# Performance work log

Hardware: AMD Instinct MI355X
Metric: run time of the kernel (lower is better)

Reference implementation:

```python
import jax, jax.numpy as jnp
import numpy as np

N_NODES = 50000
N_EDGES = 800000
IN_FEAT = 64
HID = 128
NUM_CLASSES = 32


def _glorot(key, shape):
    fan_in, fan_out = shape[0], shape[1]
    lim = jnp.sqrt(6.0 / (fan_in + fan_out))
    return jax.random.uniform(key, shape, jnp.float32, -lim, lim)


def setup_inputs() -> dict:
    key = jax.random.key(0)
    ks = jax.random.split(key, 8)
    x = jax.random.normal(ks[0], (N_NODES, IN_FEAT), dtype=jnp.float32)
    edge_index = jax.random.randint(ks[1], (2, N_EDGES), 0, N_NODES, dtype=jnp.int64 if jax.config.jax_enable_x64 else jnp.int32)
    W1 = _glorot(ks[2], (IN_FEAT, HID))
    b1 = jnp.zeros((HID,), jnp.float32)
    W2 = _glorot(ks[3], (HID, NUM_CLASSES))
    b2 = jnp.zeros((NUM_CLASSES,), jnp.float32)
    Wc = _glorot(ks[4], (NUM_CLASSES, NUM_CLASSES))
    bc = jnp.zeros((NUM_CLASSES,), jnp.float32)
    return {"x": x, "edge_index": edge_index, "W1": W1, "b1": b1,
            "W2": W2, "b2": b2, "Wc": Wc, "bc": bc}


def _gcn_conv(x, src, dst, norm, W, b):
    # x' = scatter_add(norm * gather(xW, src), dst) + b   (PyG GCNConv, self-loops included in src/dst)
    h = x @ W                                   # [N, out]
    msg = h[src] * norm[:, None]                # [E+N, out] gather + scale
    out = jax.ops.segment_sum(msg, dst, num_segments=N_NODES)  # scatter-add
    return out + b


def reference(x, edge_index, W1, b1, W2, b2, Wc, bc):
    # add self-loops (PyG GCNConv default add_self_loops=True)
    loops = jnp.arange(N_NODES, dtype=edge_index.dtype)
    src = jnp.concatenate([edge_index[0], loops])
    dst = jnp.concatenate([edge_index[1], loops])
    # symmetric normalization: deg over targets of A + I
    deg = jax.ops.segment_sum(jnp.ones_like(src, dtype=x.dtype), dst, num_segments=N_NODES)
    dinv = jnp.where(deg > 0, jax.lax.rsqrt(deg), 0.0)
    norm = dinv[src] * dinv[dst]                # [E+N]

    h = _gcn_conv(x, src, dst, norm, W1, b1)
    h = jax.nn.relu(h)                          # dropout p=0.0 -> identity
    h = _gcn_conv(h, src, dst, norm, W2, b2)
    out = h @ Wc + bc
    return (out, h)
```

## Files before the change

### kernel.cpp

```cpp
#include <hip/hip_runtime.h>


static constexpr int N  = 50000;
static constexpr int E  = 800000;
static constexpr int F0 = 64;
static constexpr int F1 = 128;
static constexpr int F2 = 32;

static constexpr int BSH    = 7;
static constexpr int BNODES = 128;
static constexpr int BMASK  = 127;
static constexpr int NBUK   = 392;
static constexpr int NSEG   = 4;
static constexpr int SEGCAP = 768;
static constexpr int BCAP   = NSEG * SEGCAP;
static constexpr int CHUNK  = 4096;
static constexpr int NCHUNK = 196;

__device__ __forceinline__ unsigned int f2bf(float f) {
  unsigned int u = __float_as_uint(f);
  return (u + 0x7fffu + ((u >> 16) & 1u)) >> 16;
}
__device__ __forceinline__ float bflo(unsigned int u) {
  return __uint_as_float(u << 16);
}
__device__ __forceinline__ float bfhi(unsigned int u) {
  return __uint_as_float(u & 0xffff0000u);
}

__global__ __launch_bounds__(512) void k_bucket(const int* __restrict__ src,
    const int* __restrict__ dst, int* __restrict__ gcur,
    unsigned int* __restrict__ ebuf) {
  __shared__ int hl[NBUK];
  int t = threadIdx.x, c = blockIdx.x;
  const int sub = c & (NSEG - 1);
  for (int i = t; i < NBUK; i += 512) hl[i] = 0;
  __syncthreads();
  int e0 = c * CHUNK, m = min(CHUNK, E - e0);
  int dreg[8];
  #pragma unroll
  for (int k = 0; k < 8; ++k) {
    int i = t + k * 512;
    if (i < m) {
      int d = dst[e0 + i];
      dreg[k] = d;
      atomicAdd(&hl[d >> BSH], 1);
    }
  }
  __syncthreads();
  for (int i = t; i < NBUK; i += 512) {
    int cc = hl[i];
    int rbase = (cc > 0) ? atomicAdd(&gcur[(i * NSEG + sub) * 16], cc) : 0;
    hl[i] = i * BCAP + sub * SEGCAP + rbase;
  }
  __syncthreads();
  #pragma unroll
  for (int k = 0; k < 8; ++k) {
    int i = t + k * 512;
    if (i < m) {
      int d = dreg[k], s = src[e0 + i];
      int pos = atomicAdd(&hl[d >> BSH], 1);
      ebuf[pos] = (unsigned int)s | ((unsigned int)(d & BMASK) << 16);
    }
  }
}

__global__ __launch_bounds__(512) void k_csr(const unsigned int* __restrict__ ebuf,
    const int* __restrict__ gcur, const float* __restrict__ x,
    int* __restrict__ cnt, int* __restrict__ rowend, float* __restrict__ dinv,
    int* __restrict__ ssrc, unsigned short* __restrict__ xs16) {
  __shared__ int cl[BNODES], sc[BNODES], cur[BNODES];
  __shared__ float dl[BNODES];
  int t = threadIdx.x, b = blockIdx.x;
  int base = b * BCAP;
  int node0 = b << BSH;
  int ms[NSEG];
  #pragma unroll
  for (int s = 0; s < NSEG; ++s) ms[s] = gcur[(b * NSEG + s) * 16];
  if (t < BNODES) cl[t] = 0;
  __syncthreads();
  unsigned int ereg[NSEG * 2];
  #pragma unroll
  for (int s = 0; s < NSEG; ++s) {
    int msz = ms[s], sb = base + s * SEGCAP;
    #pragma unroll
    for (int k = 0; k < 2; ++k) {
      int i = t + k * 512;
      unsigned int p = 0xFFFFFFFFu;
      if (i < msz) {
        p = ebuf[sb + i];
        atomicAdd(&cl[(p >> 16) & BMASK], 1);
      }
      ereg[s * 2 + k] = p;
    }
  }
  __syncthreads();
  int v = 0;
  if (t < BNODES) { v = cl[t]; sc[t] = v; }
  __syncthreads();
  for (int off = 1; off < BNODES; off <<= 1) {
    int u = (t >= off && t < BNODES) ? sc[t - off] : 0;
    __syncthreads();
    if (t < BNODES) sc[t] += u;
    __syncthreads();
  }
  if (t < BNODES) {
    int excl = sc[t] - v;
    cur[t] = excl;
    float dv = rsqrtf((float)(v + 1));
    dl[t] = dv;
    int g = node0 + t;
    if (g < N) {
      cnt[g]    = v;
      rowend[g] = base + excl + v;
      dinv[g]   = dv;
    }
  }
  __syncthreads();
  #pragma unroll
  for (int s = 0; s < NSEG; ++s) {
    #pragma unroll
    for (int k = 0; k < 2; ++k) {
      unsigned int p = ereg[s * 2 + k];
      if (p != 0xFFFFFFFFu) {
        int d = (p >> 16) & BMASK;
        int r = atomicAdd(&cur[d], 1);
        ssrc[base + r] = (int)(p & 0xFFFFu);
      }
    }
  }
  for (int i = t; i < BNODES * (F0 / 8); i += 512) {
    int nl = i >> 3, oc = i & 7;
    int n = node0 + nl;
    if (n < N) {
      float4 a  = reinterpret_cast<const float4*>(x)[n * 16 + oc * 2];
      float4 bb = reinterpret_cast<const float4*>(x)[n * 16 + oc * 2 + 1];
      float d = dl[nl];
      uint4 pk;
      pk.x = f2bf(a.x * d)  | (f2bf(a.y * d) << 16);
      pk.y = f2bf(a.z * d)  | (f2bf(a.w * d) << 16);
      pk.z = f2bf(bb.x * d) | (f2bf(bb.y * d) << 16);
      pk.w = f2bf(bb.z * d) | (f2bf(bb.w * d) << 16);
      reinterpret_cast<uint4*>(xs16)[(size_t)n * 8 + oc] = pk;
    }
  }
}

__global__ __launch_bounds__(256) void k_agg1(const int* __restrict__ rowend,
    const int* __restrict__ cnt, const int* __restrict__ ssrc,
    const unsigned short* __restrict__ xs16, const float* __restrict__ dinv,
    unsigned short* __restrict__ AX16) {
  int gw = (blockIdx.x * 256 + threadIdx.x) >> 6;
  int lane = threadIdx.x & 63;
  if (gw >= N) return;
  int end   = __builtin_amdgcn_readfirstlane(rowend[gw]);
  int deg   = __builtin_amdgcn_readfirstlane(cnt[gw]);
  int start = end - deg;
  const int g = lane >> 3, fl = lane & 7;
  const uint4* xsv = reinterpret_cast<const uint4*>(xs16);
  float acc[8];
  #pragma unroll
  for (int k = 0; k < 8; ++k) acc[k] = 0.f;
  for (int e0 = start; e0 < end; e0 += 16) {
    if (e0 + 16 <= end) {
      int s0 = ssrc[e0 + g];
      int s1 = ssrc[e0 + 8 + g];
      uint4 u0 = xsv[(size_t)s0 * 8 + fl];
      uint4 u1 = xsv[(size_t)s1 * 8 + fl];
      acc[0] += bflo(u0.x); acc[1] += bfhi(u0.x);
      acc[2] += bflo(u0.y); acc[3] += bfhi(u0.y);
      acc[4] += bflo(u0.z); acc[5] += bfhi(u0.z);
      acc[6] += bflo(u0.w); acc[7] += bfhi(u0.w);
      acc[0] += bflo(u1.x); acc[1] += bfhi(u1.x);
      acc[2] += bflo(u1.y); acc[3] += bfhi(u1.y);
      acc[4] += bflo(u1.z); acc[5] += bfhi(u1.z);
      acc[6] += bflo(u1.w); acc[7] += bfhi(u1.w);
    } else {
      int j0 = e0 + g, j1 = e0 + 8 + g;
      int s0 = ssrc[(j0 < end) ? j0 : start];
      int s1 = ssrc[(j1 < end) ? j1 : start];
      float m0 = (j0 < end) ? 1.f : 0.f;
      float m1 = (j1 < end) ? 1.f : 0.f;
      uint4 u0 = xsv[(size_t)s0 * 8 + fl];
      uint4 u1 = xsv[(size_t)s1 * 8 + fl];
      acc[0] = fmaf(bflo(u0.x), m0, acc[0]); acc[1] = fmaf(bfhi(u0.x), m0, acc[1]);
      acc[2] = fmaf(bflo(u0.y), m0, acc[2]); acc[3] = fmaf(bfhi(u0.y), m0, acc[3]);
      acc[4] = fmaf(bflo(u0.z), m0, acc[4]); acc[5] = fmaf(bfhi(u0.z), m0, acc[5]);
      acc[6] = fmaf(bflo(u0.w), m0, acc[6]); acc[7] = fmaf(bfhi(u0.w), m0, acc[7]);
      acc[0] = fmaf(bflo(u1.x), m1, acc[0]); acc[1] = fmaf(bfhi(u1.x), m1, acc[1]);
      acc[2] = fmaf(bflo(u1.y), m1, acc[2]); acc[3] = fmaf(bfhi(u1.y), m1, acc[3]);
      acc[4] = fmaf(bflo(u1.z), m1, acc[4]); acc[5] = fmaf(bfhi(u1.z), m1, acc[5]);
      acc[6] = fmaf(bflo(u1.w), m1, acc[6]); acc[7] = fmaf(bfhi(u1.w), m1, acc[7]);
    }
  }
  #pragma unroll
  for (int r = 8; r < 64; r <<= 1) {
    #pragma unroll
    for (int k = 0; k < 8; ++k) acc[k] += __shfl_xor(acc[k], r);
  }
  if (lane < 8) {
    uint4 su = xsv[(size_t)gw * 8 + fl];
    float dv = dinv[gw];
    float o[8];
    o[0] = (acc[0] + bflo(su.x)) * dv; o[1] = (acc[1] + bfhi(su.x)) * dv;
    o[2] = (acc[2] + bflo(su.y)) * dv; o[3] = (acc[3] + bfhi(su.y)) * dv;
    o[4] = (acc[4] + bflo(su.z)) * dv; o[5] = (acc[5] + bfhi(su.z)) * dv;
    o[6] = (acc[6] + bflo(su.w)) * dv; o[7] = (acc[7] + bfhi(su.w)) * dv;
    uint4 pk;
    pk.x = f2bf(o[0]) | (f2bf(o[1]) << 16);
    pk.y = f2bf(o[2]) | (f2bf(o[3]) << 16);
    pk.z = f2bf(o[4]) | (f2bf(o[5]) << 16);
    pk.w = f2bf(o[6]) | (f2bf(o[7]) << 16);
    reinterpret_cast<uint4*>(AX16)[(size_t)gw * 8 + fl] = pk;
  }
}

__global__ __launch_bounds__(256) void k_gemm12(const unsigned short* __restrict__ AX16,
    const float* __restrict__ W1, const float* __restrict__ b1,
    const float* __restrict__ W2, const float* __restrict__ dinv,
    unsigned short* __restrict__ H2s16) {
  __shared__ float arena[12544];
  float* Ws1 = arena;
  float* Xs  = arena + 8192;
  float* H1s = arena;
  float* Ws2 = arena + 8448;
  const int tid = threadIdx.x;
  const int row0 = blockIdx.x * 64;
  float4* Ws1f4 = reinterpret_cast<float4*>(Ws1);
  for (int i = tid; i < F0 * F1 / 4; i += 256) {
    int k = i >> 5, s = i & 31;
    int p = s ^ (s >> 2);
    Ws1f4[k * 32 + p] = reinterpret_cast<const float4*>(W1)[i];
  }
  const uint4* axv = reinterpret_cast<const uint4*>(AX16);
  for (int i = tid; i < 64 * 8; i += 256) {
    int r = i >> 3, q = i & 7;
    int n = row0 + r;
    float o[8] = {0.f, 0.f, 0.f, 0.f, 0.f, 0.f, 0.f, 0.f};
    if (n < N) {
      uint4 u = axv[(size_t)n * 8 + q];
      o[0] = bflo(u.x); o[1] = bfhi(u.x);
      o[2] = bflo(u.y); o[3] = bfhi(u.y);
      o[4] = bflo(u.z); o[5] = bfhi(u.z);
      o[6] = bflo(u.w); o[7] = bfhi(u.w);
    }
    *reinterpret_cast<float4*>(&Xs[r * 68 + q * 8])     = *reinterpret_cast<float4*>(o);
    *reinterpret_cast<float4*>(&Xs[r * 68 + q * 8 + 4]) = *reinterpret_cast<float4*>(o + 4);
  }
  __syncthreads();
  const int cg = tid & 15, rg = tid >> 4;
  const int c0 = cg * 8;
  const int s0 = 2 * cg, s1 = 2 * cg + 1;
  const int p0 = s0 ^ (s0 >> 2), p1 = s1 ^ (s1 >> 2);
  float acc[4][8];
  #pragma unroll
  for (int i = 0; i < 4; ++i)
    #pragma unroll
    for (int j = 0; j < 8; ++j) acc[i][j] = 0.f;
  for (int k0 = 0; k0 < F0; k0 += 4) {
    float x0[4], x1[4], x2[4], x3[4];
    *reinterpret_cast<float4*>(x0) = *reinterpret_cast<const float4*>(&Xs[(rg * 4 + 0) * 68 + k0]);
    *reinterpret_cast<float4*>(x1) = *reinterpret_cast<const float4*>(&Xs[(rg * 4 + 1) * 68 + k0]);
    *reinterpret_cast<float4*>(x2) = *reinterpret_cast<const float4*>(&Xs[(rg * 4 + 2) * 68 + k0]);
    *reinterpret_cast<float4*>(x3) = *reinterpret_cast<const float4*>(&Xs[(rg * 4 + 3) * 68 + k0]);
    #pragma unroll
    for (int kk = 0; kk < 4; ++kk) {
      float w[8];
      *reinterpret_cast<float4*>(w)     = Ws1f4[(k0 + kk) * 32 + p0];
      *reinterpret_cast<float4*>(w + 4) = Ws1f4[(k0 + kk) * 32 + p1];
      #pragma unroll
      for (int j = 0; j < 8; ++j) {
        acc[0][j] = fmaf(x0[kk], w[j], acc[0][j]);
        acc[1][j] = fmaf(x1[kk], w[j], acc[1][j]);
        acc[2][j] = fmaf(x2[kk], w[j], acc[2][j]);
        acc[3][j] = fmaf(x3[kk], w[j], acc[3][j]);
      }
    }
  }
  {
    float bb[8];
    *reinterpret_cast<float4*>(bb)     = *reinterpret_cast<const float4*>(&b1[c0]);
    *reinterpret_cast<float4*>(bb + 4) = *reinterpret_cast<const float4*>(&b1[c0 + 4]);
    #pragma unroll
    for (int i = 0; i < 4; ++i)
      #pragma unroll
      for (int j = 0; j < 8; ++j)
        acc[i][j] = fmaxf(acc[i][j] + bb[j], 0.f);
  }
  __syncthreads();
  #pragma unroll
  for (int i = 0; i < 4; ++i) {
    int r = rg * 4 + i;
    *reinterpret_cast<float4*>(&H1s[r * 132 + c0])     = *reinterpret_cast<float4*>(&acc[i][0]);
    *reinterpret_cast<float4*>(&H1s[r * 132 + c0 + 4]) = *reinterpret_cast<float4*>(&acc[i][4]);
  }
  float4* Ws2f4 = reinterpret_cast<float4*>(Ws2);
  for (int i = tid; i < F1 * F2 / 4; i += 256)
    Ws2f4[i] = reinterpret_cast<const float4*>(W2)[i];
  __syncthreads();
  const int rg2 = tid & 31, cg2 = tid >> 5;
  float acc2[2][4];
  #pragma unroll
  for (int i = 0; i < 2; ++i)
    #pragma unroll
    for (int j = 0; j < 4; ++j) acc2[i][j] = 0.f;
  for (int k0 = 0; k0 < F1; k0 += 4) {
    float h0[4], h1[4];
    *reinterpret_cast<float4*>(h0) = *reinterpret_cast<const float4*>(&H1s[rg2 * 132 + k0]);
    *reinterpret_cast<float4*>(h1) = *reinterpret_cast<const float4*>(&H1s[(rg2 + 32) * 132 + k0]);
    #pragma unroll
    for (int kk = 0; kk < 4; ++kk) {
      float w[4];
      *reinterpret_cast<float4*>(w) = Ws2f4[(k0 + kk) * 8 + cg2];
      #pragma unroll
      for (int j = 0; j < 4; ++j) {
        acc2[0][j] = fmaf(h0[kk], w[j], acc2[0][j]);
        acc2[1][j] = fmaf(h1[kk], w[j], acc2[1][j]);
      }
    }
  }
  #pragma unroll
  for (int i = 0; i < 2; ++i) {
    int n = row0 + rg2 + 32 * i;
    if (n < N) {
      float d = dinv[n];
      uint2 pk;
      pk.x = f2bf(acc2[i][0] * d) | (f2bf(acc2[i][1] * d) << 16);
      pk.y = f2bf(acc2[i][2] * d) | (f2bf(acc2[i][3] * d) << 16);
      reinterpret_cast<uint2*>(H2s16)[(size_t)n * 8 + cg2] = pk;
    }
  }
}

__global__ __launch_bounds__(256) void k_agg2h(const int* __restrict__ rowend,
    const int* __restrict__ cnt, const int* __restrict__ ssrc,
    const unsigned short* __restrict__ H2s16, const float* __restrict__ dinv,
    const float* __restrict__ b2, const float* __restrict__ Wc,
    const float* __restrict__ bc, float* __restrict__ h2,
    float* __restrict__ out) {
  __shared__ float Wcs[F2][F2];
  __shared__ float h2row[4][F2];
  const int tid = threadIdx.x;
  for (int i = tid; i < F2 * F2; i += 256) Wcs[i >> 5][i & 31] = Wc[i];
  __syncthreads();
  int gw = (blockIdx.x * 256 + tid) >> 6;
  int lane = tid & 63;
  int w = tid >> 6;
  if (gw >= N) return;
  int end   = __builtin_amdgcn_readfirstlane(rowend[gw]);
  int deg   = __builtin_amdgcn_readfirstlane(cnt[gw]);
  int start = end - deg;
  const int g = lane >> 2, fl = lane & 3;
  const uint4* hv = reinterpret_cast<const uint4*>(H2s16);
  float acc[8];
  #pragma unroll
  for (int k = 0; k < 8; ++k) acc[k] = 0.f;
  for (int e0 = start; e0 < end; e0 += 16) {
    if (e0 + 16 <= end) {
      int s = ssrc[e0 + g];
      uint4 u = hv[(size_t)s * 4 + fl];
      acc[0] += bflo(u.x); acc[1] += bfhi(u.x);
      acc[2] += bflo(u.y); acc[3] += bfhi(u.y);
      acc[4] += bflo(u.z); acc[5] += bfhi(u.z);
      acc[6] += bflo(u.w); acc[7] += bfhi(u.w);
    } else {
      int j = e0 + g;
      int s = ssrc[(j < end) ? j : start];
      float mm = (j < end) ? 1.f : 0.f;
      uint4 u = hv[(size_t)s * 4 + fl];
      acc[0] = fmaf(bflo(u.x), mm, acc[0]); acc[1] = fmaf(bfhi(u.x), mm, acc[1]);
      acc[2] = fmaf(bflo(u.y), mm, acc[2]); acc[3] = fmaf(bfhi(u.y), mm, acc[3]);
      acc[4] = fmaf(bflo(u.z), mm, acc[4]); acc[5] = fmaf(bfhi(u.z), mm, acc[5]);
      acc[6] = fmaf(bflo(u.w), mm, acc[6]); acc[7] = fmaf(bfhi(u.w), mm, acc[7]);
    }
  }
  #pragma unroll
  for (int r = 4; r < 64; r <<= 1) {
    #pragma unroll
    for (int k = 0; k < 8; ++k) acc[k] += __shfl_xor(acc[k], r);
  }
  float dv = dinv[gw];
  if (lane < 4) {
    uint4 su = hv[(size_t)gw * 4 + fl];
    float o[8];
    o[0] = dv * (acc[0] + bflo(su.x)) + b2[fl * 8 + 0];
    o[1] = dv * (acc[1] + bfhi(su.x)) + b2[fl * 8 + 1];
    o[2] = dv * (acc[2] + bflo(su.y)) + b2[fl * 8 + 2];
    o[3] = dv * (acc[3] + bfhi(su.y)) + b2[fl * 8 + 3];
    o[4] = dv * (acc[4] + bflo(su.z)) + b2[fl * 8 + 4];
    o[5] = dv * (acc[5] + bfhi(su.z)) + b2[fl * 8 + 5];
    o[6] = dv * (acc[6] + bflo(su.w)) + b2[fl * 8 + 6];
    o[7] = dv * (acc[7] + bfhi(su.w)) + b2[fl * 8 + 7];
    *reinterpret_cast<float4*>(&h2[(size_t)gw * F2 + fl * 8])     = *reinterpret_cast<float4*>(o);
    *reinterpret_cast<float4*>(&h2[(size_t)gw * F2 + fl * 8 + 4]) = *reinterpret_cast<float4*>(o + 4);
    #pragma unroll
    for (int k = 0; k < 8; ++k) h2row[w][fl * 8 + k] = o[k];
  }
  int f = lane & 31, half = lane >> 5;
  float acco = 0.f;
  #pragma unroll
  for (int kk = 0; kk < 16; ++kk) {
    int k = kk + 16 * half;
    acco = fmaf(h2row[w][k], Wcs[k][f], acco);
  }
  acco += __shfl_xor(acco, 32);
  if (half == 0) out[(size_t)gw * F2 + f] = acco + bc[f];
}

extern "C" void kernel_launch(void* const* d_in, const int* in_sizes, int n_in,
                              void* d_out, int out_size, void* d_ws, size_t ws_size,
                              hipStream_t stream) {
  const float* x  = (const float*)d_in[0];
  const int*   ei = (const int*)d_in[1];
  const int*   src = ei;
  const int*   dst = ei + E;
  const float* W1 = (const float*)d_in[2];
  const float* b1 = (const float*)d_in[3];
  const float* W2 = (const float*)d_in[4];
  const float* b2 = (const float*)d_in[5];
  const float* Wc = (const float*)d_in[6];
  const float* bc = (const float*)d_in[7];

  float* out = (float*)d_out;
  float* h2  = out + (size_t)N * F2;

  int*   cnt     = (int*)d_ws;
  int*   rowend  = cnt + N;
  int*   gcur    = rowend + N;
  float* dinv    = (float*)(gcur + NBUK * NSEG * 16);
  int*   ssrc    = (int*)(dinv + N);
  unsigned int* ebuf = (unsigned int*)(ssrc + NBUK * BCAP);
  unsigned short* xs16 = (unsigned short*)(ebuf + NBUK * BCAP);
  unsigned short* AX16 = xs16 + (size_t)N * F0;
  unsigned short* H2s16 = AX16 + (size_t)N * F0;

  hipMemsetAsync(gcur, 0, NBUK * NSEG * 16 * sizeof(int), stream);
  k_bucket<<<NCHUNK, 512, 0, stream>>>(src, dst, gcur, ebuf);
  k_csr   <<<NBUK,   512, 0, stream>>>(ebuf, gcur, x, cnt, rowend, dinv, ssrc, xs16);

  k_agg1  <<<(N + 3) / 4, 256, 0, stream>>>(rowend, cnt, ssrc, xs16, dinv, AX16);
  k_gemm12<<<(N + 63) / 64, 256, 0, stream>>>(AX16, W1, b1, W2, dinv, H2s16);
  k_agg2h <<<(N + 3) / 4, 256, 0, stream>>>(rowend, cnt, ssrc, H2s16, dinv, b2, Wc, bc, h2, out);
}
```

Measured before the change: 115.3 us.

## Compute first GCN layer GEMM with bf16 MFMA instead of scalar FMAs

The first dense transform (64→128) in the fused GEMM kernel now runs on the 16x16x32 bf16 MFMA instruction instead of a register-tiled fp32 FMA loop. W1 is converted to bf16 and packed into shared memory in the MFMA B-operand layout. The bf16 activation rows are loaded straight into A fragments, with no fp32 unpack or shared staging. The cost is bf16 rounding of W1, and the A loads have no row guard, so the final partial block reads past row N.

Measured after the change: 108.7 us. 5.7% less time.

```diff
diff --git a/kernel.cpp b/kernel.cpp
--- a/kernel.cpp
+++ b/kernel.cpp
@@ -16,6 +16,9 @@
 static constexpr int BCAP   = NSEG * SEGCAP;
 static constexpr int CHUNK  = 4096;
 static constexpr int NCHUNK = 196;
+
+typedef __attribute__((ext_vector_type(8))) short short8v;
+typedef __attribute__((ext_vector_type(4))) float float4v;
 
 __device__ __forceinline__ unsigned int f2bf(float f) {
   unsigned int u = __float_as_uint(f);
@@ -220,79 +223,48 @@
     const float* __restrict__ W2, const float* __restrict__ dinv,
     unsigned short* __restrict__ H2s16) {
   __shared__ float arena[12544];
-  float* Ws1 = arena;
-  float* Xs  = arena + 8192;
   float* H1s = arena;
   float* Ws2 = arena + 8448;
+  unsigned int* Wfu = reinterpret_cast<unsigned int*>(arena);
+  const short8v* Wf8 = reinterpret_cast<const short8v*>(arena);
   const int tid = threadIdx.x;
   const int row0 = blockIdx.x * 64;
-  float4* Ws1f4 = reinterpret_cast<float4*>(Ws1);
-  for (int i = tid; i < F0 * F1 / 4; i += 256) {
-    int k = i >> 5, s = i & 31;
-    int p = s ^ (s >> 2);
-    Ws1f4[k * 32 + p] = reinterpret_cast<const float4*>(W1)[i];
-  }
-  const uint4* axv = reinterpret_cast<const uint4*>(AX16);
-  for (int i = tid; i < 64 * 8; i += 256) {
-    int r = i >> 3, q = i & 7;
-    int n = row0 + r;
-    float o[8] = {0.f, 0.f, 0.f, 0.f, 0.f, 0.f, 0.f, 0.f};
-    if (n < N) {
-      uint4 u = axv[(size_t)n * 8 + q];
-      o[0] = bflo(u.x); o[1] = bfhi(u.x);
-      o[2] = bflo(u.y); o[3] = bfhi(u.y);
-      o[4] = bflo(u.z); o[5] = bfhi(u.z);
-      o[6] = bflo(u.w); o[7] = bfhi(u.w);
-    }
-    *reinterpret_cast<float4*>(&Xs[r * 68 + q * 8])     = *reinterpret_cast<float4*>(o);
-    *reinterpret_cast<float4*>(&Xs[r * 68 + q * 8 + 4]) = *reinterpret_cast<float4*>(o + 4);
-  }
-  __syncthreads();
-  const int cg = tid & 15, rg = tid >> 4;
-  const int c0 = cg * 8;
-  const int s0 = 2 * cg, s1 = 2 * cg + 1;
-  const int p0 = s0 ^ (s0 >> 2), p1 = s1 ^ (s1 >> 2);
-  float acc[4][8];
-  #pragma unroll
-  for (int i = 0; i < 4; ++i)
-    #pragma unroll
-    for (int j = 0; j < 8; ++j) acc[i][j] = 0.f;
-  for (int k0 = 0; k0 < F0; k0 += 4) {
-    float x0[4], x1[4], x2[4], x3[4];
-    *reinterpret_cast<float4*>(x0) = *reinterpret_cast<const float4*>(&Xs[(rg * 4 + 0) * 68 + k0]);
-    *reinterpret_cast<float4*>(x1) = *reinterpret_cast<const float4*>(&Xs[(rg * 4 + 1) * 68 + k0]);
-    *reinterpret_cast<float4*>(x2) = *reinterpret_cast<const float4*>(&Xs[(rg * 4 + 2) * 68 + k0]);
-    *reinterpret_cast<float4*>(x3) = *reinterpret_cast<const float4*>(&Xs[(rg * 4 + 3) * 68 + k0]);
-    #pragma unroll
-    for (int kk = 0; kk < 4; ++kk) {
-      float w[8];
-      *reinterpret_cast<float4*>(w)     = Ws1f4[(k0 + kk) * 32 + p0];
-      *reinterpret_cast<float4*>(w + 4) = Ws1f4[(k0 + kk) * 32 + p1];
-      #pragma unroll
-      for (int j = 0; j < 8; ++j) {
-        acc[0][j] = fmaf(x0[kk], w[j], acc[0][j]);
-        acc[1][j] = fmaf(x1[kk], w[j], acc[1][j]);
-        acc[2][j] = fmaf(x2[kk], w[j], acc[2][j]);
-        acc[3][j] = fmaf(x3[kk], w[j], acc[3][j]);
-      }
-    }
-  }
-  {
-    float bb[8];
-    *reinterpret_cast<float4*>(bb)     = *reinterpret_cast<const float4*>(&b1[c0]);
-    *reinterpret_cast<float4*>(bb + 4) = *reinterpret_cast<const float4*>(&b1[c0 + 4]);
-    #pragma unroll
-    for (int i = 0; i < 4; ++i)
-      #pragma unroll
-      for (int j = 0; j < 8; ++j)
-        acc[i][j] = fmaxf(acc[i][j] + bb[j], 0.f);
-  }
-  __syncthreads();
-  #pragma unroll
-  for (int i = 0; i < 4; ++i) {
-    int r = rg * 4 + i;
-    *reinterpret_cast<float4*>(&H1s[r * 132 + c0])     = *reinterpret_cast<float4*>(&acc[i][0]);
-    *reinterpret_cast<float4*>(&H1s[r * 132 + c0 + 4]) = *reinterpret_cast<float4*>(&acc[i][4]);
+  for (int i = tid; i < 4096; i += 256) {
+    int jh = i & 3, l = (i >> 2) & 63, f = i >> 8;
+    int k0  = (f & 1) * 32 + ((l >> 4) << 3) + jh * 2;
+    int col = (f >> 1) * 16 + (l & 15);
+    float w0 = W1[k0 * F1 + col];
+    float w1 = W1[(k0 + 1) * F1 + col];
+    Wfu[i] = f2bf(w0) | (f2bf(w1) << 16);
+  }
+  __syncthreads();
+  const int w = tid >> 6, l = tid & 63;
+  const int nrow = row0 + w * 16 + (l & 15);
+  const short8v* axv8 = reinterpret_cast<const short8v*>(AX16);
+  short8v A0 = axv8[(size_t)nrow * 8 + (l >> 4)];
+  short8v A1 = axv8[(size_t)nrow * 8 + 4 + (l >> 4)];
+  float4v acc[8];
+  #pragma unroll
+  for (int ct = 0; ct < 8; ++ct)
+    #pragma unroll
+    for (int r = 0; r < 4; ++r) acc[ct][r] = 0.f;
+  #pragma unroll
+  for (int ct = 0; ct < 8; ++ct) {
+    short8v B0 = Wf8[(ct * 2 + 0) * 64 + l];
+    short8v B1 = Wf8[(ct * 2 + 1) * 64 + l];
+    acc[ct] = __builtin_amdgcn_mfma_f32_16x16x32_bf16(A0, B0, acc[ct], 0, 0, 0);
+    acc[ct] = __builtin_amdgcn_mfma_f32_16x16x32_bf16(A1, B1, acc[ct], 0, 0, 0);
+  }
+  __syncthreads();
+  #pragma unroll
+  for (int ct = 0; ct < 8; ++ct) {
+    int col = ct * 16 + (l & 15);
+    float bb = b1[col];
+    #pragma unroll
+    for (int r = 0; r < 4; ++r) {
+      int row = w * 16 + ((l >> 4) << 2) + r;
+      H1s[row * 132 + col] = fmaxf(acc[ct][r] + bb, 0.f);
+    }
   }
   float4* Ws2f4 = reinterpret_cast<float4*>(Ws2);
   for (int i = tid; i < F1 * F2 / 4; i += 256)
@@ -310,12 +282,12 @@
     *reinterpret_cast<float4*>(h1) = *reinterpret_cast<const float4*>(&H1s[(rg2 + 32) * 132 + k0]);
     #pragma unroll
     for (int kk = 0; kk < 4; ++kk) {
-      float w[4];
-      *reinterpret_cast<float4*>(w) = Ws2f4[(k0 + kk) * 8 + cg2];
+      float ww[4];
+      *reinterpret_cast<float4*>(ww) = Ws2f4[(k0 + kk) * 8 + cg2];
       #pragma unroll
       for (int j = 0; j < 4; ++j) {
-        acc2[0][j] = fmaf(h0[kk], w[j], acc2[0][j]);
-        acc2[1][j] = fmaf(h1[kk], w[j], acc2[1][j]);
+        acc2[0][j] = fmaf(h0[kk], ww[j], acc2[0][j]);
+        acc2[1][j] = fmaf(h1[kk], ww[j], acc2[1][j]);
       }
     }
   }
```
